# Kernel optimization log

Measured on AMD Instinct MI355X. Metric: run time of the kernel, lower is better.

Reference implementation:

```python
import jax, jax.numpy as jnp
import numpy as np

N_NODES = 100000
NEG_SLOPE = 0.2  # DGL GATConv default negative_slope


def gat_layer(x, src, dst, W, attn_l, attn_r, bias, n_nodes):
    """Single-head DGL GATConv. x: [N, in], returns [N, out]."""
    h = x @ W                              # [N, out]  fc (no bias)
    el = h @ attn_l                        # [N]
    er = h @ attn_r                        # [N]
    e = el[src] + er[dst]                  # [E]
    e = jnp.where(e >= 0, e, NEG_SLOPE * e)  # leaky_relu
    # segment softmax over incoming edges of each dst node
    m = jax.ops.segment_max(e, dst, num_segments=n_nodes)   # [N]
    ex = jnp.exp(e - m[dst])                                 # [E]
    s = jax.ops.segment_sum(ex, dst, num_segments=n_nodes)  # [N]
    a = ex / s[dst]                                          # [E]
    # weighted aggregate of source features
    msg = a[:, None] * h[src]                                # [E, out]
    out = jax.ops.segment_sum(msg, dst, num_segments=n_nodes)
    return out + bias


def setup_inputs() -> dict:
    key = jax.random.key(0)
    ks = jax.random.split(key, 12)
    n, e = N_NODES, 1600000
    in_f, hid_f, out_f = 128, 64, 64
    inp = {
        "features": jax.random.normal(ks[0], (n, in_f), dtype=jnp.float32),
        "edge_weights": jax.random.uniform(ks[1], (e,), dtype=jnp.float32),
        "src": jax.random.randint(ks[2], (e,), 0, n, dtype=jnp.int32),
        "dst": jax.random.randint(ks[3], (e,), 0, n, dtype=jnp.int32),
        "W1": jax.random.normal(ks[4], (in_f, hid_f), dtype=jnp.float32) * (1.0 / np.sqrt(in_f)),
        "attn_l1": jax.random.normal(ks[5], (hid_f,), dtype=jnp.float32) * 0.1,
        "attn_r1": jax.random.normal(ks[6], (hid_f,), dtype=jnp.float32) * 0.1,
        "bias1": jnp.zeros((hid_f,), dtype=jnp.float32),
        "W2": jax.random.normal(ks[7], (hid_f, out_f), dtype=jnp.float32) * (1.0 / np.sqrt(hid_f)),
        "attn_l2": jax.random.normal(ks[8], (out_f,), dtype=jnp.float32) * 0.1,
        "attn_r2": jax.random.normal(ks[9], (out_f,), dtype=jnp.float32) * 0.1,
        "bias2": jnp.zeros((out_f,), dtype=jnp.float32),
    }
    return inp


def reference(features, edge_weights, src, dst, W1, attn_l1, attn_r1, bias1,
              W2, attn_l2, attn_r2, bias2):
    n = features.shape[0]
    # conv1 -> DGL returns [N, 1, hid]; relu; conv2 -> [N, 1, 1, out]
    h = gat_layer(features, src, dst, W1, attn_l1, attn_r1, bias1, n)  # [N, hid]
    h = jax.nn.relu(h)
    out = gat_layer(h, src, dst, W2, attn_l2, attn_r2, bias2, n)       # [N, out]
    # edge_weights is accepted but unused, matching the original forward
    return out.reshape(n, 1, 1, -1)
```

## Files before the change

### kernel.cpp

```cpp
#include <hip/hip_runtime.h>
#include <hip/hip_fp16.h>
#include <type_traits>

#define NEG_SLOPE 0.2f
#define BKT_SHIFT 8
#define BKT_SIZE (1 << BKT_SHIFT)
#define BKT_CAP 12288
#define P1_EPT 16

typedef __attribute__((ext_vector_type(8))) short short8;
typedef __attribute__((ext_vector_type(4))) float float4v;

__device__ inline int rfl_i(int v) { return __builtin_amdgcn_readfirstlane(v); }

__device__ inline unsigned short f2bf(float f) {
    unsigned u = __float_as_uint(f);
    unsigned r = u + 0x7FFFu + ((u >> 16) & 1u);
    return (unsigned short)(r >> 16);
}
__device__ inline float bf2f(unsigned short b) {
    return __uint_as_float(((unsigned)b) << 16);
}

__device__ __forceinline__ void partition_body(
        const int* __restrict__ src, const int* __restrict__ dst, int e,
        int* __restrict__ gcur, int* __restrict__ part, int nbkt, int b_id,
        char* smem) {
    int (*cnt)[392]    = (int(*)[392])smem;
    int (*base_l)[392] = (int(*)[392])(smem + 4 * 392 * sizeof(int));
    int t = threadIdx.x;
    int wv = t >> 6;
    int cb = b_id * (256 * P1_EPT);
    for (int i = t; i < 4 * 392; i += 256) ((int*)cnt)[i] = 0;
    __syncthreads();
    int sr[P1_EPT], ds[P1_EPT], rk[P1_EPT];
#pragma unroll
    for (int i4 = 0; i4 < P1_EPT / 4; ++i4) {
        int eid0 = cb + (i4 * 256 + t) * 4;
        int4 s4, d4;
        bool full = (eid0 + 3 < e);
        if (full) {
            s4 = *(const int4*)(src + eid0);
            d4 = *(const int4*)(dst + eid0);
        }
#pragma unroll
        for (int j = 0; j < 4; ++j) {
            int i = i4 * 4 + j;
            int eid = eid0 + j;
            if (full) {
                sr[i] = (&s4.x)[j];
                ds[i] = (&d4.x)[j];
            } else if (eid < e) {
                sr[i] = src[eid];
                ds[i] = dst[eid];
            }
            rk[i] = (eid < e) ? atomicAdd(&cnt[wv][ds[i] >> BKT_SHIFT], 1) : -1;
        }
    }
    __syncthreads();
    for (int b = t; b < nbkt; b += 256) {
        int c0 = cnt[0][b], c1 = cnt[1][b], c2 = cnt[2][b], c3 = cnt[3][b];
        int tot = c0 + c1 + c2 + c3;
        if (tot > 0) {
            int gb = b * BKT_CAP + atomicAdd(&gcur[b], tot);
            base_l[0][b] = gb;
            base_l[1][b] = gb + c0;
            base_l[2][b] = gb + c0 + c1;
            base_l[3][b] = gb + c0 + c1 + c2;
        }
    }
    __syncthreads();
#pragma unroll
    for (int i = 0; i < P1_EPT; ++i) {
        if (rk[i] >= 0) {
            int b = ds[i] >> BKT_SHIFT;
            part[base_l[wv][b] + rk[i]] = (sr[i] << BKT_SHIFT) | (ds[i] & (BKT_SIZE - 1));
        }
    }
}

__global__ __launch_bounds__(256) void finesort3(
        const int* __restrict__ part, const int* __restrict__ gcur,
        int* __restrict__ row_off, int* __restrict__ csr_src,
        int n, int e_total, int nbkt) {
    __shared__ int cnt[BKT_SIZE];
    __shared__ int cur[BKT_SIZE];
    __shared__ int tmp[BKT_SIZE];
    int b = blockIdx.x, t = threadIdx.x;
    int i1 = 256 + t;
    int v0 = (t < b) ? gcur[t] : 0;
    int v1 = (i1 < b) ? gcur[i1] : 0;
    tmp[t] = v0 + v1;
    __syncthreads();
    for (int o = 128; o > 0; o >>= 1) {
        if (t < o) tmp[t] += tmp[t + o];
        __syncthreads();
    }
    int bbase_b = tmp[0];
    __syncthreads();

    int d0 = b << BKT_SHIFT;
    int nloc = min(BKT_SIZE, n - d0);
    cnt[t] = 0;
    __syncthreads();
    int abase = b * BKT_CAP, aend = abase + gcur[b];
    for (int i = abase + t; i < aend; i += 256)
        atomicAdd(&cnt[part[i] & (BKT_SIZE - 1)], 1);
    __syncthreads();
    int c = cnt[t];
    tmp[t] = c;
    __syncthreads();
    for (int o = 1; o < 256; o <<= 1) {
        int x = tmp[t];
        int y = (t >= o) ? tmp[t - o] : 0;
        __syncthreads();
        tmp[t] = x + y;
        __syncthreads();
    }
    int pos0 = bbase_b + tmp[t] - c;
    cur[t] = pos0;
    if (t < nloc) row_off[d0 + t] = pos0;
    if (b == nbkt - 1 && t == 0) row_off[n] = e_total;
    __syncthreads();
    for (int i = abase + t; i < aend; i += 256) {
        int pk = part[i];
        int pos = atomicAdd(&cur[pk & (BKT_SIZE - 1)], 1);
        csr_src[pos] = ((unsigned)pk) >> BKT_SHIFT;
    }
}

template <int KT, typename IN>
__device__ __forceinline__ void gemm_body(
        const IN* __restrict__ x, const float* __restrict__ W,
        const float* __restrict__ al, const float* __restrict__ ar,
        __half* __restrict__ h16, float* __restrict__ el,
        float* __restrict__ er, int n, int bid, int nblocks, char* smem) {
    constexpr int K = KT * 32;
    constexpr int WFRAG = KT * 4 * 64 * 8;
    unsigned short* Wh = (unsigned short*)smem;
    unsigned short* Wl = Wh + WFRAG;
    for (int idx = threadIdx.x; idx < KT * 4 * 64; idx += 256) {
        int lane = idx & 63, fbkt = idx >> 6;
        int fb = fbkt & 3, kt = fbkt >> 2;
        int q = lane >> 4, c = lane & 15;
#pragma unroll
        for (int j = 0; j < 8; ++j) {
            float w = W[(kt * 32 + q * 8 + j) * 64 + fb * 16 + c];
            unsigned short hi = f2bf(w);
            Wh[idx * 8 + j] = hi;
            Wl[idx * 8 + j] = f2bf(w - bf2f(hi));
        }
    }
    __syncthreads();

    int lane = threadIdx.x & 63;
    int q = lane >> 4, c = lane & 15;
    int wave = bid * 4 + (int)(threadIdx.x >> 6);
    int nwaves = nblocks * 4;
    int ntiles = (n + 15) >> 4;

    float alv[4], arv[4];
#pragma unroll
    for (int fb = 0; fb < 4; ++fb) {
        alv[fb] = al[fb * 16 + c];
        arv[fb] = ar[fb * 16 + c];
    }

    for (int t = wave; t < ntiles; t += nwaves) {
        int v0 = t * 16;
        int row = min(v0 + c, n - 1);
        const IN* xr = x + (size_t)row * K + q * 8;

        short8 Ah[KT], Al[KT];
#pragma unroll
        for (int kt = 0; kt < KT; ++kt) {
            float xv[8];
            if constexpr (std::is_same<IN, float>::value) {
                *(float4*)&xv[0] = *(const float4*)(xr + kt * 32);
                *(float4*)&xv[4] = *(const float4*)(xr + kt * 32 + 4);
            } else {
                __half hh[8];
                *(uint4*)hh = *(const uint4*)(xr + kt * 32);
#pragma unroll
                for (int j = 0; j < 8; ++j) xv[j] = __half2float(hh[j]);
            }
#pragma unroll
            for (int j = 0; j < 8; ++j) {
                unsigned short hi = f2bf(xv[j]);
                Ah[kt][j] = (short)hi;
                Al[kt][j] = (short)f2bf(xv[j] - bf2f(hi));
            }
        }

        float4v acc[4];
#pragma unroll
        for (int fb = 0; fb < 4; ++fb) acc[fb] = (float4v)0.f;

#pragma unroll
        for (int kt = 0; kt < KT; ++kt) {
#pragma unroll
            for (int fb = 0; fb < 4; ++fb) {
                short8 bh = *(const short8*)&Wh[((kt * 4 + fb) * 64 + lane) * 8];
                short8 bl = *(const short8*)&Wl[((kt * 4 + fb) * 64 + lane) * 8];
                acc[fb] = __builtin_amdgcn_mfma_f32_16x16x32_bf16(Ah[kt], bh, acc[fb], 0, 0, 0);
                acc[fb] = __builtin_amdgcn_mfma_f32_16x16x32_bf16(Al[kt], bh, acc[fb], 0, 0, 0);
                acc[fb] = __builtin_amdgcn_mfma_f32_16x16x32_bf16(Ah[kt], bl, acc[fb], 0, 0, 0);
            }
        }

#pragma unroll
        for (int r = 0; r < 4; ++r) {
            int v = v0 + q * 4 + r;
            float pl = 0.f, pr = 0.f;
            bool ok = (v < n);
#pragma unroll
            for (int fb = 0; fb < 4; ++fb) {
                float hv = acc[fb][r];
                if (ok) h16[(size_t)v * 64 + fb * 16 + c] = __float2half(hv);
                pl = fmaf(hv, alv[fb], pl);
                pr = fmaf(hv, arv[fb], pr);
            }
#pragma unroll
            for (int off = 8; off > 0; off >>= 1) {
                pl += __shfl_xor(pl, off);
                pr += __shfl_xor(pr, off);
            }
            if (ok && c == 0) { el[v] = pl; er[v] = pr; }
        }
    }
}

__global__ __launch_bounds__(256) void part_gemm1(
        const int* __restrict__ src, const int* __restrict__ dst, int e,
        int* __restrict__ gcur, int* __restrict__ part, int nbkt, int npb,
        const float* __restrict__ x, const float* __restrict__ W1,
        const float* __restrict__ al, const float* __restrict__ ar,
        __half* __restrict__ h16, float* __restrict__ el,
        float* __restrict__ er, int n) {
    __shared__ char smem[32768];
    int b = (int)blockIdx.x;
    if (b < npb)
        partition_body(src, dst, e, gcur, part, nbkt, b, smem);
    else
        gemm_body<4, float>(x, W1, al, ar, h16, el, er, n, b - npb,
                            (int)gridDim.x - npb, smem);
}

template <int KT, typename IN>
__global__ __launch_bounds__(256) void gemm_mfma_kernel(
        const IN* __restrict__ x, const float* __restrict__ W,
        const float* __restrict__ al, const float* __restrict__ ar,
        __half* __restrict__ h16, float* __restrict__ el,
        float* __restrict__ er, int n) {
    __shared__ char smem[KT * 4 * 64 * 8 * 2 * 2];
    gemm_body<KT, IN>(x, W, al, ar, h16, el, er, n, (int)blockIdx.x,
                      (int)gridDim.x, smem);
}

template <typename OUT>
__global__ __launch_bounds__(256) void agg_kernel(
        const int* __restrict__ row_off, const int* __restrict__ csr_src,
        const __half* __restrict__ h16, const float* __restrict__ el,
        const float* __restrict__ er, const float* __restrict__ bias,
        OUT* __restrict__ out, int n, int do_relu) {
    int lane = threadIdx.x & 63;
    int grp = lane >> 4;
    int c = lane & 15;
    int gwave = rfl_i((int)((blockIdx.x * blockDim.x + threadIdx.x) >> 6));
    int nwaves = (gridDim.x * blockDim.x) >> 6;
    float4 b4 = ((const float4*)bias)[c];
    for (int v = gwave; v < n; v += nwaves) {
        int rs = rfl_i(row_off[v]), re = rfl_i(row_off[v + 1]);
        float er_v = er[v];
        float a0 = 0.f, a1 = 0.f, a2 = 0.f, a3 = 0.f, ssum = 0.f;
        for (int base = rs; base < re; base += 64) {
            int cnt = min(64, re - base);
            int s_e = 0;
            float ex = 0.f;
            if (lane < cnt) {
                s_e = csr_src[base + lane];
                float ev = el[s_e] + er_v;
                ev = (ev >= 0.f) ? ev : NEG_SLOPE * ev;
                ex = __expf(ev);
            }
            float cs = ex;
#pragma unroll
            for (int off = 32; off > 0; off >>= 1) cs += __shfl_xor(cs, off);
            ssum += cs;
            int cnt16 = (cnt + 15) & ~15;
            for (int j = 0; j < cnt16; j += 16) {
                int sj[4];
                float exj[4];
                uint2 hv[4];
#pragma unroll
                for (int u = 0; u < 4; ++u) {
                    int idx = j + 4 * u + grp;
                    sj[u] = __shfl(s_e, idx);
                    exj[u] = __shfl(ex, idx);
                    hv[u] = *((const uint2*)(h16 + (size_t)sj[u] * 64) + c);
                }
#pragma unroll
                for (int u = 0; u < 4; ++u) {
                    float2 f01 = __half22float2(*(__half2*)&hv[u].x);
                    float2 f23 = __half22float2(*(__half2*)&hv[u].y);
                    a0 = fmaf(exj[u], f01.x, a0);
                    a1 = fmaf(exj[u], f01.y, a1);
                    a2 = fmaf(exj[u], f23.x, a2);
                    a3 = fmaf(exj[u], f23.y, a3);
                }
            }
        }
#pragma unroll
        for (int off = 16; off < 64; off <<= 1) {
            a0 += __shfl_xor(a0, off);
            a1 += __shfl_xor(a1, off);
            a2 += __shfl_xor(a2, off);
            a3 += __shfl_xor(a3, off);
        }
        if (lane < 16) {
            float4 o;
            if (re > rs) {
                float inv = 1.0f / ssum;
                o.x = fmaf(a0, inv, b4.x);
                o.y = fmaf(a1, inv, b4.y);
                o.z = fmaf(a2, inv, b4.z);
                o.w = fmaf(a3, inv, b4.w);
            } else {
                o = b4;
            }
            if (do_relu) {
                o.x = fmaxf(o.x, 0.f);
                o.y = fmaxf(o.y, 0.f);
                o.z = fmaxf(o.z, 0.f);
                o.w = fmaxf(o.w, 0.f);
            }
            if constexpr (std::is_same<OUT, __half>::value) {
                uint2 pk;
                *(__half2*)&pk.x = __float22half2_rn(make_float2(o.x, o.y));
                *(__half2*)&pk.y = __float22half2_rn(make_float2(o.z, o.w));
                ((uint2*)(out + (size_t)v * 64))[c] = pk;
            } else {
                ((float4*)(out + (size_t)v * 64))[c] = o;
            }
        }
    }
}

extern "C" void kernel_launch(void* const* d_in, const int* in_sizes, int n_in,
                              void* d_out, int out_size, void* d_ws, size_t ws_size,
                              hipStream_t stream) {
    (void)n_in; (void)out_size; (void)ws_size;
    const float* features = (const float*)d_in[0];
    const int*   src = (const int*)d_in[2];
    const int*   dst = (const int*)d_in[3];
    const float* W1  = (const float*)d_in[4];
    const float* al1 = (const float*)d_in[5];
    const float* ar1 = (const float*)d_in[6];
    const float* b1  = (const float*)d_in[7];
    const float* W2  = (const float*)d_in[8];
    const float* al2 = (const float*)d_in[9];
    const float* ar2 = (const float*)d_in[10];
    const float* b2  = (const float*)d_in[11];

    const int n = in_sizes[0] / 128;
    const int e = in_sizes[2];
    float* out = (float*)d_out;

    char* p = (char*)d_ws;
    auto alloc = [&](size_t bytes) -> char* {
        char* q = p;
        p += (bytes + 255) & ~(size_t)255;
        return q;
    };
    int*    row_off = (int*)alloc((size_t)(n + 1) * 4);
    int*    csr_src = (int*)alloc((size_t)e * 4);
    __half* h16     = (__half*)alloc((size_t)n * 64 * 2);
    __half* hr      = (__half*)alloc((size_t)n * 64 * 2);
    float*  el      = (float*)alloc((size_t)n * 4);
    float*  er      = (float*)alloc((size_t)n * 4);
    int*    gcur    = (int*)alloc(512 * 4);
    int*    part    = (int*)d_out;

    const int nbkt = (n + BKT_SIZE - 1) >> BKT_SHIFT;
    const int npb  = (e + 256 * P1_EPT - 1) / (256 * P1_EPT);

    hipMemsetAsync(gcur, 0, 512 * sizeof(int), stream);

    part_gemm1<<<npb + 512, 256, 0, stream>>>(src, dst, e, gcur, part, nbkt, npb,
                                              features, W1, al1, ar1, h16, el, er, n);
    finesort3<<<nbkt, 256, 0, stream>>>(part, gcur, row_off, csr_src, n, e, nbkt);

    agg_kernel<__half><<<4096, 256, 0, stream>>>(row_off, csr_src, h16, el, er, b1, hr, n, 1);

    gemm_mfma_kernel<2, __half><<<512, 256, 0, stream>>>(hr, W2, al2, ar2, h16, el, er, n);
    agg_kernel<float><<<4096, 256, 0, stream>>>(row_off, csr_src, h16, el, er, b2, out, n, 0);
}
```

Before: 244.3 us.

## Store node features in 8-wide feature slices and aggregate per slice

Changes the layout of the half-precision node features from row-major [N,64] to eight slices of [N,8]. The GEMM now writes this layout, the second GEMM reads its input in it, and the aggregation kernel is rewritten so each block handles one slice and each half-wave handles one destination node with one edge per lane. The goal is a smaller working set per slice, so gathered rows stay cache-resident, and to drop the shuffle-heavy per-edge broadcast loop. In exchange, the edge softmax weights (el lookups and exp) are recomputed in each of the eight slices, and the final output writes become strided.

```diff
diff --git a/kernel.cpp b/kernel.cpp
--- a/kernel.cpp
+++ b/kernel.cpp
@@ -129,11 +129,11 @@
     }
 }
 
-template <int KT, typename IN>
+template <int KT, typename IN, bool SLICED_IN>
 __device__ __forceinline__ void gemm_body(
         const IN* __restrict__ x, const float* __restrict__ W,
         const float* __restrict__ al, const float* __restrict__ ar,
-        __half* __restrict__ h16, float* __restrict__ el,
+        __half* __restrict__ hs, float* __restrict__ el,
         float* __restrict__ er, int n, int bid, int nblocks, char* smem) {
     constexpr int K = KT * 32;
     constexpr int WFRAG = KT * 4 * 64 * 8;
@@ -169,18 +169,19 @@
     for (int t = wave; t < ntiles; t += nwaves) {
         int v0 = t * 16;
         int row = min(v0 + c, n - 1);
-        const IN* xr = x + (size_t)row * K + q * 8;
 
         short8 Ah[KT], Al[KT];
 #pragma unroll
         for (int kt = 0; kt < KT; ++kt) {
             float xv[8];
-            if constexpr (std::is_same<IN, float>::value) {
-                *(float4*)&xv[0] = *(const float4*)(xr + kt * 32);
-                *(float4*)&xv[4] = *(const float4*)(xr + kt * 32 + 4);
+            if constexpr (!SLICED_IN) {
+                const IN* xp = x + (size_t)row * K + kt * 32 + q * 8;
+                *(float4*)&xv[0] = *(const float4*)xp;
+                *(float4*)&xv[4] = *(const float4*)(xp + 4);
             } else {
+                const IN* xp = x + ((size_t)(kt * 4 + q) * n + row) * 8;
                 __half hh[8];
-                *(uint4*)hh = *(const uint4*)(xr + kt * 32);
+                *(uint4*)hh = *(const uint4*)xp;
 #pragma unroll
                 for (int j = 0; j < 8; ++j) xv[j] = __half2float(hh[j]);
             }
@@ -216,7 +217,10 @@
 #pragma unroll
             for (int fb = 0; fb < 4; ++fb) {
                 float hv = acc[fb][r];
-                if (ok) h16[(size_t)v * 64 + fb * 16 + c] = __float2half(hv);
+                if (ok) {
+                    size_t off = ((size_t)(fb * 2 + (c >> 3)) * n + v) * 8 + (c & 7);
+                    hs[off] = __float2half(hv);
+                }
                 pl = fmaf(hv, alv[fb], pl);
                 pr = fmaf(hv, arv[fb], pr);
             }
@@ -235,112 +239,108 @@
         int* __restrict__ gcur, int* __restrict__ part, int nbkt, int npb,
         const float* __restrict__ x, const float* __restrict__ W1,
         const float* __restrict__ al, const float* __restrict__ ar,
-        __half* __restrict__ h16, float* __restrict__ el,
+        __half* __restrict__ hs, float* __restrict__ el,
         float* __restrict__ er, int n) {
     __shared__ char smem[32768];
     int b = (int)blockIdx.x;
     if (b < npb)
         partition_body(src, dst, e, gcur, part, nbkt, b, smem);
     else
-        gemm_body<4, float>(x, W1, al, ar, h16, el, er, n, b - npb,
-                            (int)gridDim.x - npb, smem);
-}
-
-template <int KT, typename IN>
+        gemm_body<4, float, false>(x, W1, al, ar, hs, el, er, n, b - npb,
+                                   (int)gridDim.x - npb, smem);
+}
+
+template <int KT, typename IN, bool SLICED_IN>
 __global__ __launch_bounds__(256) void gemm_mfma_kernel(
         const IN* __restrict__ x, const float* __restrict__ W,
         const float* __restrict__ al, const float* __restrict__ ar,
-        __half* __restrict__ h16, float* __restrict__ el,
+        __half* __restrict__ hs, float* __restrict__ el,
         float* __restrict__ er, int n) {
     __shared__ char smem[KT * 4 * 64 * 8 * 2 * 2];
-    gemm_body<KT, IN>(x, W, al, ar, h16, el, er, n, (int)blockIdx.x,
-                      (int)gridDim.x, smem);
+    gemm_body<KT, IN, SLICED_IN>(x, W, al, ar, hs, el, er, n, (int)blockIdx.x,
+                                 (int)gridDim.x, smem);
 }
 
 template <typename OUT>
-__global__ __launch_bounds__(256) void agg_kernel(
+__global__ __launch_bounds__(256) void agg_sliced(
         const int* __restrict__ row_off, const int* __restrict__ csr_src,
-        const __half* __restrict__ h16, const float* __restrict__ el,
+        const __half* __restrict__ hs, const float* __restrict__ el,
         const float* __restrict__ er, const float* __restrict__ bias,
         OUT* __restrict__ out, int n, int do_relu) {
     int lane = threadIdx.x & 63;
-    int grp = lane >> 4;
-    int c = lane & 15;
-    int gwave = rfl_i((int)((blockIdx.x * blockDim.x + threadIdx.x) >> 6));
-    int nwaves = (gridDim.x * blockDim.x) >> 6;
-    float4 b4 = ((const float4*)bias)[c];
-    for (int v = gwave; v < n; v += nwaves) {
-        int rs = rfl_i(row_off[v]), re = rfl_i(row_off[v + 1]);
-        float er_v = er[v];
-        float a0 = 0.f, a1 = 0.f, a2 = 0.f, a3 = 0.f, ssum = 0.f;
-        for (int base = rs; base < re; base += 64) {
-            int cnt = min(64, re - base);
-            int s_e = 0;
+    int g = lane >> 5;
+    int l = lane & 31;
+    int slice = blockIdx.x & 7;
+    int wave = ((int)blockIdx.x >> 3) * 4 + (int)(threadIdx.x >> 6);
+    int nwps = ((int)gridDim.x >> 3) * 4;
+    const __half* __restrict__ hsl = hs + (size_t)slice * n * 8;
+
+    float bf[8];
+    *(float4*)&bf[0] = ((const float4*)bias)[slice * 2];
+    *(float4*)&bf[4] = ((const float4*)bias)[slice * 2 + 1];
+
+    for (int v0 = wave * 2; v0 < n; v0 += nwps * 2) {
+        int v = v0 + g;
+        bool act = (v < n);
+        int vc = act ? v : (n - 1);
+        int rs = row_off[vc];
+        int re = act ? row_off[vc + 1] : rs;
+        float er_v = er[vc];
+
+        float acc[8];
+#pragma unroll
+        for (int f = 0; f < 8; ++f) acc[f] = 0.f;
+        float ssum = 0.f;
+
+        for (int base = rs; base < re; base += 32) {
+            int idx = base + l;
+            bool on = (idx < re);
+            int s_e = on ? csr_src[idx] : 0;
+            uint4 hv = make_uint4(0, 0, 0, 0);
             float ex = 0.f;
-            if (lane < cnt) {
-                s_e = csr_src[base + lane];
+            if (on) {
+                hv = *(const uint4*)(hsl + (size_t)s_e * 8);
                 float ev = el[s_e] + er_v;
                 ev = (ev >= 0.f) ? ev : NEG_SLOPE * ev;
                 ex = __expf(ev);
             }
-            float cs = ex;
-#pragma unroll
-            for (int off = 32; off > 0; off >>= 1) cs += __shfl_xor(cs, off);
-            ssum += cs;
-            int cnt16 = (cnt + 15) & ~15;
-            for (int j = 0; j < cnt16; j += 16) {
-                int sj[4];
-                float exj[4];
-                uint2 hv[4];
-#pragma unroll
-                for (int u = 0; u < 4; ++u) {
-                    int idx = j + 4 * u + grp;
-                    sj[u] = __shfl(s_e, idx);
-                    exj[u] = __shfl(ex, idx);
-                    hv[u] = *((const uint2*)(h16 + (size_t)sj[u] * 64) + c);
-                }
-#pragma unroll
-                for (int u = 0; u < 4; ++u) {
-                    float2 f01 = __half22float2(*(__half2*)&hv[u].x);
-                    float2 f23 = __half22float2(*(__half2*)&hv[u].y);
-                    a0 = fmaf(exj[u], f01.x, a0);
-                    a1 = fmaf(exj[u], f01.y, a1);
-                    a2 = fmaf(exj[u], f23.x, a2);
-                    a3 = fmaf(exj[u], f23.y, a3);
-                }
-            }
-        }
-#pragma unroll
-        for (int off = 16; off < 64; off <<= 1) {
-            a0 += __shfl_xor(a0, off);
-            a1 += __shfl_xor(a1, off);
-            a2 += __shfl_xor(a2, off);
-            a3 += __shfl_xor(a3, off);
-        }
-        if (lane < 16) {
-            float4 o;
-            if (re > rs) {
-                float inv = 1.0f / ssum;
-                o.x = fmaf(a0, inv, b4.x);
-                o.y = fmaf(a1, inv, b4.y);
-                o.z = fmaf(a2, inv, b4.z);
-                o.w = fmaf(a3, inv, b4.w);
+            ssum += ex;
+            __half2* hp = (__half2*)&hv;
+#pragma unroll
+            for (int f2 = 0; f2 < 4; ++f2) {
+                float2 ff = __half22float2(hp[f2]);
+                acc[2 * f2]     = fmaf(ex, ff.x, acc[2 * f2]);
+                acc[2 * f2 + 1] = fmaf(ex, ff.y, acc[2 * f2 + 1]);
+            }
+        }
+
+#pragma unroll
+        for (int off = 16; off >= 1; off >>= 1) {
+            ssum += __shfl_xor(ssum, off);
+#pragma unroll
+            for (int f = 0; f < 8; ++f) acc[f] += __shfl_xor(acc[f], off);
+        }
+
+        if (act && l == 0) {
+            bool has = (re > rs);
+            float inv = has ? 1.0f / ssum : 0.f;
+            float o[8];
+#pragma unroll
+            for (int f = 0; f < 8; ++f) {
+                o[f] = has ? fmaf(acc[f], inv, bf[f]) : bf[f];
+                if (do_relu) o[f] = fmaxf(o[f], 0.f);
+            }
+            if constexpr (std::is_same<OUT, __half>::value) {
+                uint4 pk;
+                __half2* pp = (__half2*)&pk;
+#pragma unroll
+                for (int f2 = 0; f2 < 4; ++f2)
+                    pp[f2] = __float22half2_rn(make_float2(o[2 * f2], o[2 * f2 + 1]));
+                *(uint4*)(out + ((size_t)slice * n + v) * 8) = pk;
             } else {
-                o = b4;
-            }
-            if (do_relu) {
-                o.x = fmaxf(o.x, 0.f);
-                o.y = fmaxf(o.y, 0.f);
-                o.z = fmaxf(o.z, 0.f);
-                o.w = fmaxf(o.w, 0.f);
-            }
-            if constexpr (std::is_same<OUT, __half>::value) {
-                uint2 pk;
-                *(__half2*)&pk.x = __float22half2_rn(make_float2(o.x, o.y));
-                *(__half2*)&pk.y = __float22half2_rn(make_float2(o.z, o.w));
-                ((uint2*)(out + (size_t)v * 64))[c] = pk;
-            } else {
-                ((float4*)(out + (size_t)v * 64))[c] = o;
+                float4* op = (float4*)(out + (size_t)v * 64 + slice * 8);
+                op[0] = make_float4(o[0], o[1], o[2], o[3]);
+                op[1] = make_float4(o[4], o[5], o[6], o[7]);
             }
         }
     }
@@ -390,8 +390,9 @@
                                               features, W1, al1, ar1, h16, el, er, n);
     finesort3<<<nbkt, 256, 0, stream>>>(part, gcur, row_off, csr_src, n, e, nbkt);
 
-    agg_kernel<__half><<<4096, 256, 0, stream>>>(row_off, csr_src, h16, el, er, b1, hr, n, 1);
-
-    gemm_mfma_kernel<2, __half><<<512, 256, 0, stream>>>(hr, W2, al2, ar2, h16, el, er, n);
-    agg_kernel<float><<<4096, 256, 0, stream>>>(row_off, csr_src, h16, el, er, b2, out, n, 0);
-}
+    agg_sliced<__half><<<2048, 256, 0, stream>>>(row_off, csr_src, h16, el, er, b1, hr, n, 1);
+
+    gemm_mfma_kernel<2, __half, true><<<512, 256, 0, stream>>>(hr, W2, al2, ar2,
+                                                               h16, el, er, n);
+    agg_sliced<float><<<2048, 256, 0, stream>>>(row_off, csr_src, h16, el, er, b2, out, n, 0);
+}
```

Measured after the change: 579.7 us. 137% more time.

## Replace bucket partition plus fine sort with global histogram, scan, and atomic scatter

Applied to the files above, without the earlier changes.

CSR construction changes from a two-pass bucketed partition (coarse buckets in an intermediate buffer, then a per-bucket LDS fine sort) to a per-node global atomic histogram, a scan over buckets and nodes, and a scatter that places each edge with a global atomic on a per-node cursor. This drops the intermediate packed partition buffer and its second read pass. In exchange it issues many global atomics on a 100k-entry array, reads src and dst again in a separate kernel, and adds a kernel launch and a larger memset. Edge order within each row is now nondeterministic, which can slightly change float summation order.

```diff
diff --git a/kernel.cpp b/kernel.cpp
--- a/kernel.cpp
+++ b/kernel.cpp
@@ -5,7 +5,6 @@
 #define NEG_SLOPE 0.2f
 #define BKT_SHIFT 8
 #define BKT_SIZE (1 << BKT_SHIFT)
-#define BKT_CAP 12288
 #define P1_EPT 16
 
 typedef __attribute__((ext_vector_type(8))) short short8;
@@ -22,18 +21,83 @@
     return __uint_as_float(((unsigned)b) << 16);
 }
 
-__device__ __forceinline__ void partition_body(
-        const int* __restrict__ src, const int* __restrict__ dst, int e,
-        int* __restrict__ gcur, int* __restrict__ part, int nbkt, int b_id,
+__device__ __forceinline__ void hist_body(
+        const int* __restrict__ dst, int e,
+        int* __restrict__ hist, int* __restrict__ gbkt, int nbkt, int b_id,
         char* smem) {
-    int (*cnt)[392]    = (int(*)[392])smem;
-    int (*base_l)[392] = (int(*)[392])(smem + 4 * 392 * sizeof(int));
+    int (*cnt)[392] = (int(*)[392])smem;
     int t = threadIdx.x;
     int wv = t >> 6;
     int cb = b_id * (256 * P1_EPT);
     for (int i = t; i < 4 * 392; i += 256) ((int*)cnt)[i] = 0;
     __syncthreads();
-    int sr[P1_EPT], ds[P1_EPT], rk[P1_EPT];
+#pragma unroll
+    for (int i4 = 0; i4 < P1_EPT / 4; ++i4) {
+        int eid0 = cb + (i4 * 256 + t) * 4;
+        int4 d4;
+        bool full = (eid0 + 3 < e);
+        if (full) d4 = *(const int4*)(dst + eid0);
+#pragma unroll
+        for (int j = 0; j < 4; ++j) {
+            int eid = eid0 + j;
+            int d;
+            if (full) d = (&d4.x)[j];
+            else if (eid < e) d = dst[eid];
+            else continue;
+            atomicAdd(&hist[d], 1);
+            atomicAdd(&cnt[wv][d >> BKT_SHIFT], 1);
+        }
+    }
+    __syncthreads();
+    for (int b = t; b < nbkt; b += 256) {
+        int tot = cnt[0][b] + cnt[1][b] + cnt[2][b] + cnt[3][b];
+        if (tot > 0) atomicAdd(&gbkt[b], tot);
+    }
+}
+
+__global__ __launch_bounds__(256) void scan_kernel(
+        const int* __restrict__ hist, const int* __restrict__ gbkt,
+        int* __restrict__ row_off, int* __restrict__ cur,
+        int n, int e_total, int nbkt) {
+    __shared__ int tmp[256];
+    int b = blockIdx.x, t = threadIdx.x;
+    int i1 = 256 + t;
+    int v0 = (t < b) ? gbkt[t] : 0;
+    int v1 = (i1 < b) ? gbkt[i1] : 0;
+    tmp[t] = v0 + v1;
+    __syncthreads();
+    for (int o = 128; o > 0; o >>= 1) {
+        if (t < o) tmp[t] += tmp[t + o];
+        __syncthreads();
+    }
+    int bbase_b = tmp[0];
+    __syncthreads();
+
+    int d0 = b << BKT_SHIFT;
+    int nloc = min(BKT_SIZE, n - d0);
+    int c = (t < nloc) ? hist[d0 + t] : 0;
+    tmp[t] = c;
+    __syncthreads();
+    for (int o = 1; o < 256; o <<= 1) {
+        int x = tmp[t];
+        int y = (t >= o) ? tmp[t - o] : 0;
+        __syncthreads();
+        tmp[t] = x + y;
+        __syncthreads();
+    }
+    int pos0 = bbase_b + tmp[t] - c;
+    if (t < nloc) {
+        row_off[d0 + t] = pos0;
+        cur[d0 + t] = pos0;
+    }
+    if (b == nbkt - 1 && t == 0) row_off[n] = e_total;
+}
+
+__global__ __launch_bounds__(256) void scatter_kernel(
+        const int* __restrict__ src, const int* __restrict__ dst, int e,
+        int* __restrict__ cur, int* __restrict__ csr_src) {
+    int t = threadIdx.x;
+    int cb = (int)blockIdx.x * (256 * P1_EPT);
 #pragma unroll
     for (int i4 = 0; i4 < P1_EPT / 4; ++i4) {
         int eid0 = cb + (i4 * 256 + t) * 4;
@@ -45,87 +109,20 @@
         }
 #pragma unroll
         for (int j = 0; j < 4; ++j) {
-            int i = i4 * 4 + j;
             int eid = eid0 + j;
+            int s, d;
             if (full) {
-                sr[i] = (&s4.x)[j];
-                ds[i] = (&d4.x)[j];
+                s = (&s4.x)[j];
+                d = (&d4.x)[j];
             } else if (eid < e) {
-                sr[i] = src[eid];
-                ds[i] = dst[eid];
-            }
-            rk[i] = (eid < e) ? atomicAdd(&cnt[wv][ds[i] >> BKT_SHIFT], 1) : -1;
-        }
-    }
-    __syncthreads();
-    for (int b = t; b < nbkt; b += 256) {
-        int c0 = cnt[0][b], c1 = cnt[1][b], c2 = cnt[2][b], c3 = cnt[3][b];
-        int tot = c0 + c1 + c2 + c3;
-        if (tot > 0) {
-            int gb = b * BKT_CAP + atomicAdd(&gcur[b], tot);
-            base_l[0][b] = gb;
-            base_l[1][b] = gb + c0;
-            base_l[2][b] = gb + c0 + c1;
-            base_l[3][b] = gb + c0 + c1 + c2;
-        }
-    }
-    __syncthreads();
-#pragma unroll
-    for (int i = 0; i < P1_EPT; ++i) {
-        if (rk[i] >= 0) {
-            int b = ds[i] >> BKT_SHIFT;
-            part[base_l[wv][b] + rk[i]] = (sr[i] << BKT_SHIFT) | (ds[i] & (BKT_SIZE - 1));
-        }
-    }
-}
-
-__global__ __launch_bounds__(256) void finesort3(
-        const int* __restrict__ part, const int* __restrict__ gcur,
-        int* __restrict__ row_off, int* __restrict__ csr_src,
-        int n, int e_total, int nbkt) {
-    __shared__ int cnt[BKT_SIZE];
-    __shared__ int cur[BKT_SIZE];
-    __shared__ int tmp[BKT_SIZE];
-    int b = blockIdx.x, t = threadIdx.x;
-    int i1 = 256 + t;
-    int v0 = (t < b) ? gcur[t] : 0;
-    int v1 = (i1 < b) ? gcur[i1] : 0;
-    tmp[t] = v0 + v1;
-    __syncthreads();
-    for (int o = 128; o > 0; o >>= 1) {
-        if (t < o) tmp[t] += tmp[t + o];
-        __syncthreads();
-    }
-    int bbase_b = tmp[0];
-    __syncthreads();
-
-    int d0 = b << BKT_SHIFT;
-    int nloc = min(BKT_SIZE, n - d0);
-    cnt[t] = 0;
-    __syncthreads();
-    int abase = b * BKT_CAP, aend = abase + gcur[b];
-    for (int i = abase + t; i < aend; i += 256)
-        atomicAdd(&cnt[part[i] & (BKT_SIZE - 1)], 1);
-    __syncthreads();
-    int c = cnt[t];
-    tmp[t] = c;
-    __syncthreads();
-    for (int o = 1; o < 256; o <<= 1) {
-        int x = tmp[t];
-        int y = (t >= o) ? tmp[t - o] : 0;
-        __syncthreads();
-        tmp[t] = x + y;
-        __syncthreads();
-    }
-    int pos0 = bbase_b + tmp[t] - c;
-    cur[t] = pos0;
-    if (t < nloc) row_off[d0 + t] = pos0;
-    if (b == nbkt - 1 && t == 0) row_off[n] = e_total;
-    __syncthreads();
-    for (int i = abase + t; i < aend; i += 256) {
-        int pk = part[i];
-        int pos = atomicAdd(&cur[pk & (BKT_SIZE - 1)], 1);
-        csr_src[pos] = ((unsigned)pk) >> BKT_SHIFT;
+                s = src[eid];
+                d = dst[eid];
+            } else {
+                continue;
+            }
+            int pos = atomicAdd(&cur[d], 1);
+            csr_src[pos] = s;
+        }
     }
 }
 
@@ -230,9 +227,9 @@
     }
 }
 
-__global__ __launch_bounds__(256) void part_gemm1(
-        const int* __restrict__ src, const int* __restrict__ dst, int e,
-        int* __restrict__ gcur, int* __restrict__ part, int nbkt, int npb,
+__global__ __launch_bounds__(256) void hist_gemm1(
+        const int* __restrict__ dst, int e,
+        int* __restrict__ hist, int* __restrict__ gbkt, int nbkt, int npb,
         const float* __restrict__ x, const float* __restrict__ W1,
         const float* __restrict__ al, const float* __restrict__ ar,
         __half* __restrict__ h16, float* __restrict__ el,
@@ -240,7 +237,7 @@
     __shared__ char smem[32768];
     int b = (int)blockIdx.x;
     if (b < npb)
-        partition_body(src, dst, e, gcur, part, nbkt, b, smem);
+        hist_body(dst, e, hist, gbkt, nbkt, b, smem);
     else
         gemm_body<4, float>(x, W1, al, ar, h16, el, er, n, b - npb,
                             (int)gridDim.x - npb, smem);
@@ -378,17 +375,19 @@
     __half* hr      = (__half*)alloc((size_t)n * 64 * 2);
     float*  el      = (float*)alloc((size_t)n * 4);
     float*  er      = (float*)alloc((size_t)n * 4);
-    int*    gcur    = (int*)alloc(512 * 4);
-    int*    part    = (int*)d_out;
+    int*    hist    = (int*)alloc((size_t)(n + 512) * 4);
+    int*    gbkt    = hist + n;
+    int*    cur     = (int*)alloc((size_t)n * 4);
 
     const int nbkt = (n + BKT_SIZE - 1) >> BKT_SHIFT;
     const int npb  = (e + 256 * P1_EPT - 1) / (256 * P1_EPT);
 
-    hipMemsetAsync(gcur, 0, 512 * sizeof(int), stream);
-
-    part_gemm1<<<npb + 512, 256, 0, stream>>>(src, dst, e, gcur, part, nbkt, npb,
+    hipMemsetAsync(hist, 0, (size_t)(n + 512) * 4, stream);
+
+    hist_gemm1<<<npb + 512, 256, 0, stream>>>(dst, e, hist, gbkt, nbkt, npb,
                                               features, W1, al1, ar1, h16, el, er, n);
-    finesort3<<<nbkt, 256, 0, stream>>>(part, gcur, row_off, csr_src, n, e, nbkt);
+    scan_kernel<<<nbkt, 256, 0, stream>>>(hist, gbkt, row_off, cur, n, e, nbkt);
+    scatter_kernel<<<npb, 256, 0, stream>>>(src, dst, e, cur, csr_src);
 
     agg_kernel<__half><<<4096, 256, 0, stream>>>(row_off, csr_src, h16, el, er, b1, hr, n, 1);
 
```

Result: slower. 410.8 us (+68.2%).

## Replace atomic bucket partition with fixed-slot layout and fuse GEMM2 into aggregation

Applied to the files above, without the earlier changes.

Partition blocks now write edges into fixed per-(bucket, block) slots and record their counts, which removes the global atomic cursor and its memset. The fine sort prefix-scans those counts, stages each bucket in LDS and emits separate row_beg/row_end arrays into a padded CSR. The second-layer linear transform is fused into the first aggregation using an LDS-resident W2 and shuffles, which drops the half-precision intermediate round trip and one launch. The fixed capacities (96 per slot, 6144 per bucket) silently drop edges on skewed graphs, and the sparse padded part buffer costs extra memory traffic.

```diff
diff --git a/kernel.cpp b/kernel.cpp
--- a/kernel.cpp
+++ b/kernel.cpp
@@ -5,7 +5,9 @@
 #define NEG_SLOPE 0.2f
 #define BKT_SHIFT 8
 #define BKT_SIZE (1 << BKT_SHIFT)
-#define BKT_CAP 12288
+#define NPB_PAD 400
+#define SCAP 96
+#define BCAP 6144
 #define P1_EPT 16
 
 typedef __attribute__((ext_vector_type(8))) short short8;
@@ -24,13 +26,13 @@
 
 __device__ __forceinline__ void partition_body(
         const int* __restrict__ src, const int* __restrict__ dst, int e,
-        int* __restrict__ gcur, int* __restrict__ part, int nbkt, int b_id,
-        char* smem) {
+        int* __restrict__ part, int* __restrict__ cnts2, int nbkt, int npb,
+        int blk, char* smem) {
     int (*cnt)[392]    = (int(*)[392])smem;
     int (*base_l)[392] = (int(*)[392])(smem + 4 * 392 * sizeof(int));
     int t = threadIdx.x;
     int wv = t >> 6;
-    int cb = b_id * (256 * P1_EPT);
+    int cb = blk * (256 * P1_EPT);
     for (int i = t; i < 4 * 392; i += 256) ((int*)cnt)[i] = 0;
     __syncthreads();
     int sr[P1_EPT], ds[P1_EPT], rk[P1_EPT];
@@ -61,54 +63,39 @@
     for (int b = t; b < nbkt; b += 256) {
         int c0 = cnt[0][b], c1 = cnt[1][b], c2 = cnt[2][b], c3 = cnt[3][b];
         int tot = c0 + c1 + c2 + c3;
-        if (tot > 0) {
-            int gb = b * BKT_CAP + atomicAdd(&gcur[b], tot);
-            base_l[0][b] = gb;
-            base_l[1][b] = gb + c0;
-            base_l[2][b] = gb + c0 + c1;
-            base_l[3][b] = gb + c0 + c1 + c2;
-        }
+        base_l[0][b] = 0;
+        base_l[1][b] = c0;
+        base_l[2][b] = c0 + c1;
+        base_l[3][b] = c0 + c1 + c2;
+        cnts2[b * NPB_PAD + blk] = min(tot, SCAP);
     }
     __syncthreads();
 #pragma unroll
     for (int i = 0; i < P1_EPT; ++i) {
         if (rk[i] >= 0) {
             int b = ds[i] >> BKT_SHIFT;
-            part[base_l[wv][b] + rk[i]] = (sr[i] << BKT_SHIFT) | (ds[i] & (BKT_SIZE - 1));
-        }
-    }
-}
-
-__global__ __launch_bounds__(256) void finesort3(
-        const int* __restrict__ part, const int* __restrict__ gcur,
-        int* __restrict__ row_off, int* __restrict__ csr_src,
-        int n, int e_total, int nbkt) {
-    __shared__ int cnt[BKT_SIZE];
-    __shared__ int cur[BKT_SIZE];
-    __shared__ int tmp[BKT_SIZE];
+            int o = base_l[wv][b] + rk[i];
+            if (o < SCAP)
+                part[((size_t)b * NPB_PAD + blk) * SCAP + o] =
+                    (sr[i] << BKT_SHIFT) | (ds[i] & (BKT_SIZE - 1));
+        }
+    }
+}
+
+__global__ __launch_bounds__(256) void finesort4(
+        const int* __restrict__ part, const int* __restrict__ cnts2,
+        int* __restrict__ row_beg, int* __restrict__ row_end,
+        int* __restrict__ csr_src, int n, int nbkt, int npb) {
+    __shared__ int cnt[256];
+    __shared__ int cur[256];
+    __shared__ int tmp[256];
+    __shared__ int stage[BCAP];
     int b = blockIdx.x, t = threadIdx.x;
-    int i1 = 256 + t;
-    int v0 = (t < b) ? gcur[t] : 0;
-    int v1 = (i1 < b) ? gcur[i1] : 0;
-    tmp[t] = v0 + v1;
-    __syncthreads();
-    for (int o = 128; o > 0; o >>= 1) {
-        if (t < o) tmp[t] += tmp[t + o];
-        __syncthreads();
-    }
-    int bbase_b = tmp[0];
-    __syncthreads();
-
-    int d0 = b << BKT_SHIFT;
-    int nloc = min(BKT_SIZE, n - d0);
-    cnt[t] = 0;
-    __syncthreads();
-    int abase = b * BKT_CAP, aend = abase + gcur[b];
-    for (int i = abase + t; i < aend; i += 256)
-        atomicAdd(&cnt[part[i] & (BKT_SIZE - 1)], 1);
-    __syncthreads();
-    int c = cnt[t];
-    tmp[t] = c;
+    int blk0 = 2 * t, blk1 = 2 * t + 1;
+    int c0 = (blk0 < npb) ? cnts2[b * NPB_PAD + blk0] : 0;
+    int c1 = (blk1 < npb) ? cnts2[b * NPB_PAD + blk1] : 0;
+    int s = c0 + c1;
+    tmp[t] = s;
     __syncthreads();
     for (int o = 1; o < 256; o <<= 1) {
         int x = tmp[t];
@@ -117,24 +104,59 @@
         tmp[t] = x + y;
         __syncthreads();
     }
-    int pos0 = bbase_b + tmp[t] - c;
+    int excl = tmp[t] - s;
+    int S = tmp[255];
+    int Seff = min(S, BCAP);
+    {
+        const int* sp0 = part + ((size_t)b * NPB_PAD + blk0) * SCAP;
+        for (int i = 0; i < c0; ++i) {
+            int p = excl + i;
+            if (p < BCAP) stage[p] = sp0[i];
+        }
+        const int* sp1 = part + ((size_t)b * NPB_PAD + blk1) * SCAP;
+        int sb1 = excl + c0;
+        for (int i = 0; i < c1; ++i) {
+            int p = sb1 + i;
+            if (p < BCAP) stage[p] = sp1[i];
+        }
+    }
+    cnt[t] = 0;
+    __syncthreads();
+    for (int i = t; i < Seff; i += 256)
+        atomicAdd(&cnt[stage[i] & (BKT_SIZE - 1)], 1);
+    __syncthreads();
+    int d0 = b << BKT_SHIFT;
+    int nloc = min(BKT_SIZE, n - d0);
+    int c = cnt[t];
+    tmp[t] = c;
+    __syncthreads();
+    for (int o = 1; o < 256; o <<= 1) {
+        int x = tmp[t];
+        int y = (t >= o) ? tmp[t - o] : 0;
+        __syncthreads();
+        tmp[t] = x + y;
+        __syncthreads();
+    }
+    int pos0 = b * BCAP + tmp[t] - c;
     cur[t] = pos0;
-    if (t < nloc) row_off[d0 + t] = pos0;
-    if (b == nbkt - 1 && t == 0) row_off[n] = e_total;
-    __syncthreads();
-    for (int i = abase + t; i < aend; i += 256) {
-        int pk = part[i];
+    if (t < nloc) {
+        row_beg[d0 + t] = pos0;
+        row_end[d0 + t] = pos0 + c;
+    }
+    __syncthreads();
+    for (int i = t; i < Seff; i += 256) {
+        int pk = stage[i];
         int pos = atomicAdd(&cur[pk & (BKT_SIZE - 1)], 1);
         csr_src[pos] = ((unsigned)pk) >> BKT_SHIFT;
     }
 }
 
-template <int KT, typename IN>
 __device__ __forceinline__ void gemm_body(
-        const IN* __restrict__ x, const float* __restrict__ W,
+        const float* __restrict__ x, const float* __restrict__ W,
         const float* __restrict__ al, const float* __restrict__ ar,
         __half* __restrict__ h16, float* __restrict__ el,
         float* __restrict__ er, int n, int bid, int nblocks, char* smem) {
+    constexpr int KT = 4;
     constexpr int K = KT * 32;
     constexpr int WFRAG = KT * 4 * 64 * 8;
     unsigned short* Wh = (unsigned short*)smem;
@@ -169,21 +191,14 @@
     for (int t = wave; t < ntiles; t += nwaves) {
         int v0 = t * 16;
         int row = min(v0 + c, n - 1);
-        const IN* xr = x + (size_t)row * K + q * 8;
+        const float* xr = x + (size_t)row * K + q * 8;
 
         short8 Ah[KT], Al[KT];
 #pragma unroll
         for (int kt = 0; kt < KT; ++kt) {
             float xv[8];
-            if constexpr (std::is_same<IN, float>::value) {
-                *(float4*)&xv[0] = *(const float4*)(xr + kt * 32);
-                *(float4*)&xv[4] = *(const float4*)(xr + kt * 32 + 4);
-            } else {
-                __half hh[8];
-                *(uint4*)hh = *(const uint4*)(xr + kt * 32);
-#pragma unroll
-                for (int j = 0; j < 8; ++j) xv[j] = __half2float(hh[j]);
-            }
+            *(float4*)&xv[0] = *(const float4*)(xr + kt * 32);
+            *(float4*)&xv[4] = *(const float4*)(xr + kt * 32 + 4);
 #pragma unroll
             for (int j = 0; j < 8; ++j) {
                 unsigned short hi = f2bf(xv[j]);
@@ -232,7 +247,7 @@
 
 __global__ __launch_bounds__(256) void part_gemm1(
         const int* __restrict__ src, const int* __restrict__ dst, int e,
-        int* __restrict__ gcur, int* __restrict__ part, int nbkt, int npb,
+        int* __restrict__ part, int* __restrict__ cnts2, int nbkt, int npb,
         const float* __restrict__ x, const float* __restrict__ W1,
         const float* __restrict__ al, const float* __restrict__ ar,
         __half* __restrict__ h16, float* __restrict__ el,
@@ -240,37 +255,35 @@
     __shared__ char smem[32768];
     int b = (int)blockIdx.x;
     if (b < npb)
-        partition_body(src, dst, e, gcur, part, nbkt, b, smem);
+        partition_body(src, dst, e, part, cnts2, nbkt, npb, b, smem);
     else
-        gemm_body<4, float>(x, W1, al, ar, h16, el, er, n, b - npb,
-                            (int)gridDim.x - npb, smem);
-}
-
-template <int KT, typename IN>
-__global__ __launch_bounds__(256) void gemm_mfma_kernel(
-        const IN* __restrict__ x, const float* __restrict__ W,
-        const float* __restrict__ al, const float* __restrict__ ar,
-        __half* __restrict__ h16, float* __restrict__ el,
-        float* __restrict__ er, int n) {
-    __shared__ char smem[KT * 4 * 64 * 8 * 2 * 2];
-    gemm_body<KT, IN>(x, W, al, ar, h16, el, er, n, (int)blockIdx.x,
-                      (int)gridDim.x, smem);
-}
-
-template <typename OUT>
-__global__ __launch_bounds__(256) void agg_kernel(
-        const int* __restrict__ row_off, const int* __restrict__ csr_src,
-        const __half* __restrict__ h16, const float* __restrict__ el,
-        const float* __restrict__ er, const float* __restrict__ bias,
-        OUT* __restrict__ out, int n, int do_relu) {
+        gemm_body(x, W1, al, ar, h16, el, er, n, b - npb,
+                  (int)gridDim.x - npb, smem);
+}
+
+__global__ __launch_bounds__(256) void agg_gemm2(
+        const int* __restrict__ row_beg, const int* __restrict__ row_end,
+        const int* __restrict__ csr_src, const __half* __restrict__ h16,
+        const float* __restrict__ el, const float* __restrict__ er,
+        const float* __restrict__ bias1, const float* __restrict__ W2,
+        const float* __restrict__ al2, const float* __restrict__ ar2,
+        __half* __restrict__ h2out, float* __restrict__ el2,
+        float* __restrict__ er2, int n) {
+    __shared__ float W2L[4096];
+    for (int i = threadIdx.x; i < 1024; i += 256)
+        ((float4*)W2L)[i] = ((const float4*)W2)[i];
+    __syncthreads();
+
     int lane = threadIdx.x & 63;
     int grp = lane >> 4;
     int c = lane & 15;
     int gwave = rfl_i((int)((blockIdx.x * blockDim.x + threadIdx.x) >> 6));
     int nwaves = (gridDim.x * blockDim.x) >> 6;
-    float4 b4 = ((const float4*)bias)[c];
+    float4 b4 = ((const float4*)bias1)[c];
+    float alv2 = al2[lane], arv2 = ar2[lane];
+
     for (int v = gwave; v < n; v += nwaves) {
-        int rs = rfl_i(row_off[v]), re = rfl_i(row_off[v + 1]);
+        int rs = rfl_i(row_beg[v]), re = rfl_i(row_end[v]);
         float er_v = er[v];
         float a0 = 0.f, a1 = 0.f, a2 = 0.f, a3 = 0.f, ssum = 0.f;
         for (int base = rs; base < re; base += 64) {
@@ -317,6 +330,103 @@
             a2 += __shfl_xor(a2, off);
             a3 += __shfl_xor(a3, off);
         }
+        float4 o;
+        if (re > rs) {
+            float inv = 1.0f / ssum;
+            o.x = fmaf(a0, inv, b4.x);
+            o.y = fmaf(a1, inv, b4.y);
+            o.z = fmaf(a2, inv, b4.z);
+            o.w = fmaf(a3, inv, b4.w);
+        } else {
+            o = b4;
+        }
+        o.x = fmaxf(o.x, 0.f);
+        o.y = fmaxf(o.y, 0.f);
+        o.z = fmaxf(o.z, 0.f);
+        o.w = fmaxf(o.w, 0.f);
+
+        float acc2 = 0.f;
+#pragma unroll
+        for (int k4 = 0; k4 < 16; ++k4) {
+            float vx = __shfl(o.x, k4);
+            float vy = __shfl(o.y, k4);
+            float vz = __shfl(o.z, k4);
+            float vw = __shfl(o.w, k4);
+            acc2 = fmaf(vx, W2L[(4 * k4 + 0) * 64 + lane], acc2);
+            acc2 = fmaf(vy, W2L[(4 * k4 + 1) * 64 + lane], acc2);
+            acc2 = fmaf(vz, W2L[(4 * k4 + 2) * 64 + lane], acc2);
+            acc2 = fmaf(vw, W2L[(4 * k4 + 3) * 64 + lane], acc2);
+        }
+        h2out[(size_t)v * 64 + lane] = __float2half(acc2);
+        float pl = acc2 * alv2, pr = acc2 * arv2;
+#pragma unroll
+        for (int off = 32; off > 0; off >>= 1) {
+            pl += __shfl_xor(pl, off);
+            pr += __shfl_xor(pr, off);
+        }
+        if (lane == 0) { el2[v] = pl; er2[v] = pr; }
+    }
+}
+
+__global__ __launch_bounds__(256) void agg_final(
+        const int* __restrict__ row_beg, const int* __restrict__ row_end,
+        const int* __restrict__ csr_src, const __half* __restrict__ h2,
+        const float* __restrict__ el2, const float* __restrict__ er2,
+        const float* __restrict__ bias2, float* __restrict__ out, int n) {
+    int lane = threadIdx.x & 63;
+    int grp = lane >> 4;
+    int c = lane & 15;
+    int gwave = rfl_i((int)((blockIdx.x * blockDim.x + threadIdx.x) >> 6));
+    int nwaves = (gridDim.x * blockDim.x) >> 6;
+    float4 b4 = ((const float4*)bias2)[c];
+    for (int v = gwave; v < n; v += nwaves) {
+        int rs = rfl_i(row_beg[v]), re = rfl_i(row_end[v]);
+        float er_v = er2[v];
+        float a0 = 0.f, a1 = 0.f, a2 = 0.f, a3 = 0.f, ssum = 0.f;
+        for (int base = rs; base < re; base += 64) {
+            int cnt = min(64, re - base);
+            int s_e = 0;
+            float ex = 0.f;
+            if (lane < cnt) {
+                s_e = csr_src[base + lane];
+                float ev = el2[s_e] + er_v;
+                ev = (ev >= 0.f) ? ev : NEG_SLOPE * ev;
+                ex = __expf(ev);
+            }
+            float cs = ex;
+#pragma unroll
+            for (int off = 32; off > 0; off >>= 1) cs += __shfl_xor(cs, off);
+            ssum += cs;
+            int cnt16 = (cnt + 15) & ~15;
+            for (int j = 0; j < cnt16; j += 16) {
+                int sj[4];
+                float exj[4];
+                uint2 hv[4];
+#pragma unroll
+                for (int u = 0; u < 4; ++u) {
+                    int idx = j + 4 * u + grp;
+                    sj[u] = __shfl(s_e, idx);
+                    exj[u] = __shfl(ex, idx);
+                    hv[u] = *((const uint2*)(h2 + (size_t)sj[u] * 64) + c);
+                }
+#pragma unroll
+                for (int u = 0; u < 4; ++u) {
+                    float2 f01 = __half22float2(*(__half2*)&hv[u].x);
+                    float2 f23 = __half22float2(*(__half2*)&hv[u].y);
+                    a0 = fmaf(exj[u], f01.x, a0);
+                    a1 = fmaf(exj[u], f01.y, a1);
+                    a2 = fmaf(exj[u], f23.x, a2);
+                    a3 = fmaf(exj[u], f23.y, a3);
+                }
+            }
+        }
+#pragma unroll
+        for (int off = 16; off < 64; off <<= 1) {
+            a0 += __shfl_xor(a0, off);
+            a1 += __shfl_xor(a1, off);
+            a2 += __shfl_xor(a2, off);
+            a3 += __shfl_xor(a3, off);
+        }
         if (lane < 16) {
             float4 o;
             if (re > rs) {
@@ -328,20 +438,7 @@
             } else {
                 o = b4;
             }
-            if (do_relu) {
-                o.x = fmaxf(o.x, 0.f);
-                o.y = fmaxf(o.y, 0.f);
-                o.z = fmaxf(o.z, 0.f);
-                o.w = fmaxf(o.w, 0.f);
-            }
-            if constexpr (std::is_same<OUT, __half>::value) {
-                uint2 pk;
-                *(__half2*)&pk.x = __float22half2_rn(make_float2(o.x, o.y));
-                *(__half2*)&pk.y = __float22half2_rn(make_float2(o.z, o.w));
-                ((uint2*)(out + (size_t)v * 64))[c] = pk;
-            } else {
-                ((float4*)(out + (size_t)v * 64))[c] = o;
-            }
+            ((float4*)(out + (size_t)v * 64))[c] = o;
         }
     }
 }
@@ -372,26 +469,27 @@
         p += (bytes + 255) & ~(size_t)255;
         return q;
     };
-    int*    row_off = (int*)alloc((size_t)(n + 1) * 4);
-    int*    csr_src = (int*)alloc((size_t)e * 4);
+    const int nbkt = (n + BKT_SIZE - 1) >> BKT_SHIFT;
+    const int npb  = (e + 256 * P1_EPT - 1) / (256 * P1_EPT);
+
+    int*    row_beg = (int*)alloc((size_t)n * 4);
+    int*    row_end = (int*)alloc((size_t)n * 4);
+    int*    csr_src = (int*)alloc((size_t)nbkt * BCAP * 4);
     __half* h16     = (__half*)alloc((size_t)n * 64 * 2);
-    __half* hr      = (__half*)alloc((size_t)n * 64 * 2);
+    __half* h2      = (__half*)alloc((size_t)n * 64 * 2);
     float*  el      = (float*)alloc((size_t)n * 4);
     float*  er      = (float*)alloc((size_t)n * 4);
-    int*    gcur    = (int*)alloc(512 * 4);
-    int*    part    = (int*)d_out;
-
-    const int nbkt = (n + BKT_SIZE - 1) >> BKT_SHIFT;
-    const int npb  = (e + 256 * P1_EPT - 1) / (256 * P1_EPT);
-
-    hipMemsetAsync(gcur, 0, 512 * sizeof(int), stream);
-
-    part_gemm1<<<npb + 512, 256, 0, stream>>>(src, dst, e, gcur, part, nbkt, npb,
+    float*  el2     = (float*)alloc((size_t)n * 4);
+    float*  er2     = (float*)alloc((size_t)n * 4);
+    int*    cnts2   = (int*)alloc((size_t)nbkt * NPB_PAD * 4);
+    int*    part    = (int*)alloc((size_t)nbkt * NPB_PAD * SCAP * 4);
+
+    part_gemm1<<<npb + 512, 256, 0, stream>>>(src, dst, e, part, cnts2, nbkt, npb,
                                               features, W1, al1, ar1, h16, el, er, n);
-    finesort3<<<nbkt, 256, 0, stream>>>(part, gcur, row_off, csr_src, n, e, nbkt);
-
-    agg_kernel<__half><<<4096, 256, 0, stream>>>(row_off, csr_src, h16, el, er, b1, hr, n, 1);
-
-    gemm_mfma_kernel<2, __half><<<512, 256, 0, stream>>>(hr, W2, al2, ar2, h16, el, er, n);
-    agg_kernel<float><<<4096, 256, 0, stream>>>(row_off, csr_src, h16, el, er, b2, out, n, 0);
-}
+    finesort4<<<nbkt, 256, 0, stream>>>(part, cnts2, row_beg, row_end, csr_src,
+                                        n, nbkt, npb);
+    agg_gemm2<<<4096, 256, 0, stream>>>(row_beg, row_end, csr_src, h16, el, er,
+                                        b1, W2, al2, ar2, h2, el2, er2, n);
+    agg_final<<<4096, 256, 0, stream>>>(row_beg, row_end, csr_src, h2, el2, er2,
+                                        b2, out, n);
+}
```

Result: slower. 310.3 us (+27.0%).
